# Optimization experiments

Hardware: AMD Instinct MI355X
Metric: run time of the kernel (lower is better)

The kernel has to match this reference:

```python
import jax, jax.numpy as jnp
import numpy as np
import math

D_MODEL = 1024
N_HEADS = 16
FACTOR = 5


def setup_inputs() -> dict:
    key = jax.random.key(0)
    ks = jax.random.split(key, 8)
    B, L, S, d = 8, 4096, 4096, D_MODEL
    sc = 1.0 / math.sqrt(d)
    perm = jnp.asarray(np.random.default_rng(0).permutation(L), jnp.int32)
    return {
        "queries": jax.random.normal(ks[0], (B, L, d), jnp.float32),
        "keys": jax.random.normal(ks[1], (B, S, d), jnp.float32),
        "values": jax.random.normal(ks[2], (B, S, d), jnp.float32),
        "perm": perm,
        "Wq": jax.random.normal(ks[3], (d, d), jnp.float32) * sc,
        "bq": jnp.zeros((d,), jnp.float32),
        "Wk": jax.random.normal(ks[4], (d, d), jnp.float32) * sc,
        "bk": jnp.zeros((d,), jnp.float32),
        "Wv": jax.random.normal(ks[5], (d, d), jnp.float32) * sc,
        "bv": jnp.zeros((d,), jnp.float32),
        "Wo": jax.random.normal(ks[6], (d, d), jnp.float32) * sc,
        "bo": jnp.zeros((d,), jnp.float32),
    }


def reference(queries, keys, values, perm, Wq, bq, Wk, bk, Wv, bv, Wo, bo):
    B, L, d = queries.shape
    S = keys.shape[1]
    H = N_HEADS
    dk = d // H

    q = (queries @ Wq + bq).reshape(B, L, H, dk)
    k = (keys @ Wk + bk).reshape(B, S, H, dk)
    v = (values @ Wv + bv).reshape(B, S, H, dk)

    # ProbSparse: u = min(factor * ceil(log(S)), L)  (static, shape-derived)
    u_part = FACTOR * int(math.ceil(math.log(S)))
    u = min(u_part, L)

    # sample u queries (perm replaces torch.randperm for determinism)
    q_sample = q[:, perm[:u]]                                   # [B,u,H,dk]
    scores_sample = jnp.einsum('buhd,bshd->bhus', q_sample, k)  # [B,H,u,S]

    # sparsity measurement M = max_s - mean_s
    M = scores_sample.max(-1) - scores_sample.sum(-1) / S       # [B,H,u]
    _, M_top = jax.lax.top_k(M, u)                              # [B,H,u] indices in [0,u)

    # gather top-u queries per (batch, head) along the L axis
    qT = q.transpose(0, 2, 1, 3)                                # [B,H,L,dk]
    q_red = jnp.take_along_axis(qT, M_top[..., None], axis=2)   # [B,H,u,dk]

    scores = jnp.einsum('bhud,bshd->bhus', q_red, k)            # [B,H,u,S]
    attn = jax.nn.softmax(scores, axis=-1)
    context = jnp.einsum('bhus,bshd->buhd', attn, v).reshape(B, u, d)
    output = context @ Wo + bo                                  # [B,u,d]
    return output, attn
```

## Files before the change

kernel.cpp:

```cpp
#include <hip/hip_runtime.h>
#include <stdint.h>
#include <stddef.h>

#define DEV static __device__ __forceinline__

typedef short short8 __attribute__((ext_vector_type(8)));
typedef short short4v __attribute__((ext_vector_type(4)));
typedef float f32x4 __attribute__((ext_vector_type(4)));
typedef _Float16 half8 __attribute__((ext_vector_type(8)));

DEV uint16_t f2h(float x){
  union { _Float16 h; uint16_t u; } c; c.h = (_Float16)x; return c.u;
}

DEV f32x4 mfma16h(short8 a, short8 b, f32x4 c){
  union { short8 s; half8 h; } ua, ub; ua.s = a; ub.s = b;
  return __builtin_amdgcn_mfma_f32_16x16x32_f16(ua.h, ub.h, c, 0, 0, 0);
}

typedef const __attribute__((address_space(1))) void* gas1;
typedef __attribute__((address_space(3))) void* las3;
DEV void async16(const void* g, void* l){
  __builtin_amdgcn_global_load_lds((gas1)g, (las3)l, 16, 0, 0);
}

DEV int swzoct(int row, int oct){ return (oct & ~7) | ((oct ^ row) & 7); }
DEV short8 lds_frag(const short* base, int row, int rowOcts, int oct){
  int o = swzoct(row, oct);
  return *(const short8*)(base + row * rowOcts * 8 + o * 8);
}
DEV void lds_store8(short* base, int row, int rowOcts, int oct, short8 v){
  int o = swzoct(row, oct);
  *(short8*)(base + row * rowOcts * 8 + o * 8) = v;
}

__global__ __launch_bounds__(256) void pa_prep_weights(
    const float* __restrict__ Wk, const float* __restrict__ Wv,
    uint16_t* WkT, uint16_t* WvT){
  int which = blockIdx.y;
  const float* W = which ? Wv : Wk;
  uint16_t* O = which ? WvT : WkT;
  int e0 = (blockIdx.x * 256 + threadIdx.x) * 4;
  #pragma unroll
  for(int c=0;c<4;c++){
    int e = e0 + c; int n = e >> 10, k = e & 1023;
    O[e] = f2h(W[(size_t)k*1024 + n]);
  }
}

__global__ __launch_bounds__(256) void pa_prep_inputs(
    const float* __restrict__ keys, const float* __restrict__ values,
    uint16_t* __restrict__ kf, uint16_t* __restrict__ vf){
  size_t e = ((size_t)blockIdx.x * 256 + threadIdx.x) * 8;
  const float* src = blockIdx.y ? values : keys;
  uint16_t* dst = blockIdx.y ? vf : kf;
  float4 u0 = *(const float4*)(src + e);
  float4 u1 = *(const float4*)(src + e + 4);
  float xs[8] = {u0.x,u0.y,u0.z,u0.w,u1.x,u1.y,u1.z,u1.w};
  short8 hv;
  #pragma unroll
  for(int c=0;c<8;c++) hv[c] = (short)f2h(xs[c]);
  *(short8*)(dst + e) = hv;
}

__global__ __launch_bounds__(256) void pa_q_stage1(
    const float* __restrict__ queries, const int* __restrict__ perm,
    const float* __restrict__ Wq, double* __restrict__ qpart){
  __shared__ alignas(16) float Alds[96*32];
  __shared__ alignas(16) float Blds[32*128];
  int ct = blockIdx.x, kc = blockIdx.y, b = blockIdx.z;
  int t = threadIdx.x;
  int tr = t >> 4, tc = t & 15;
  const float* qb = queries + (size_t)b*4096*1024;
  const float* srcA[3];
  #pragma unroll
  for(int rr=0; rr<3; rr++){
    int chunk = rr*256 + t;
    int row = chunk >> 3, c8 = chunk & 7;
    int rid = (row < 45) ? perm[row] : (row < 90 ? row - 45 : 0);
    srcA[rr] = qb + (size_t)rid*1024 + c8*4;
  }
  const float* srcB[4];
  #pragma unroll
  for(int rr=0; rr<4; rr++){
    int chunk = rr*256 + t;
    int kk = chunk >> 5, c = chunk & 31;
    srcB[rr] = Wq + (size_t)kk*1024 + ct*128 + c*4;
  }
  double acc[6][8];
  #pragma unroll
  for(int i=0;i<6;i++)
    #pragma unroll
    for(int jj=0;jj<8;jj++) acc[i][jj] = 0.0;
  int k0 = kc*128;
  for(int ks=0; ks<4; ks++){
    int kk0 = k0 + ks*32;
    #pragma unroll
    for(int rr=0; rr<3; rr++)
      async16(srcA[rr] + kk0, (char*)Alds + (rr*256 + t)*16);
    #pragma unroll
    for(int rr=0; rr<4; rr++)
      async16(srcB[rr] + (size_t)kk0*1024, (char*)Blds + (rr*256 + t)*16);
    __syncthreads();
    #pragma unroll
    for(int kk=0; kk<32; kk++){
      double av[6];
      #pragma unroll
      for(int i=0;i<6;i++) av[i] = (double)Alds[(tr*6+i)*32 + kk];
      float4 b0 = *(const float4*)(Blds + kk*128 + tc*8);
      float4 b1 = *(const float4*)(Blds + kk*128 + tc*8 + 4);
      double bv[8] = {(double)b0.x,(double)b0.y,(double)b0.z,(double)b0.w,
                      (double)b1.x,(double)b1.y,(double)b1.z,(double)b1.w};
      #pragma unroll
      for(int i=0;i<6;i++)
        #pragma unroll
        for(int jj=0;jj<8;jj++)
          acc[i][jj] += av[i]*bv[jj];
    }
    __syncthreads();
  }
  #pragma unroll
  for(int i=0;i<6;i++){
    int r = tr*6 + i;
    double* dst = qpart + (((size_t)b*96 + r)*8 + kc)*1024 + ct*128 + tc*8;
    #pragma unroll
    for(int jj=0;jj<8;jj++) dst[jj] = acc[i][jj];
  }
}

__global__ __launch_bounds__(256) void pa_q_finalize(
    const double* __restrict__ qpart, const float* __restrict__ bq,
    float* q_f32, uint16_t* q_f16){
  int slot = blockIdx.x, b = blockIdx.y;
  int j = (slot < 45) ? slot : ((slot >= 48 && slot < 93) ? (45 + slot - 48) : -1);
  #pragma unroll
  for(int c=0;c<4;c++){
    int n = threadIdx.x * 4 + c;
    float v = 0.f;
    if(j >= 0){
      const double* p = qpart + (((size_t)b*96 + j)*8)*1024 + n;
      double s = 0.0;
      #pragma unroll
      for(int kc=0;kc<8;kc++) s += p[(size_t)kc*1024];
      v = (float)(s + (double)bq[n]);
    }
    int h = n >> 6, d = n & 63;
    size_t idx = (((size_t)(b*16 + h))*96 + slot)*64 + d;
    q_f32[idx] = v;
    q_f16[idx] = f2h(v);
  }
}

template<bool TR>
__global__ __launch_bounds__(256) void pa_kv_gemm(
    const uint16_t* __restrict__ Ag, const uint16_t* __restrict__ Bg,
    const float* __restrict__ bias, uint16_t* __restrict__ out){
  __shared__ alignas(16) short Ah[128*64], Bh[128*64];
  int tid = threadIdx.x, wid = tid >> 6, lane = tid & 63;
  int bid = blockIdx.x;
  int xcd = bid & 7, slot = bid >> 3;
  int mt = xcd*32 + (slot >> 3), nt = slot & 7;
  int m0 = mt*128, n0 = nt*128;
  int rsub = lane >> 3;
  int soct = (lane & 7) ^ rsub;
  const uint16_t* a0 = Ag + (size_t)(m0 + wid*32 + rsub)*1024 + soct*8;
  const uint16_t* b0 = Bg + (size_t)(n0 + wid*32 + rsub)*1024 + soct*8;
  short* lA = Ah + wid*32*64;
  short* lB = Bh + wid*32*64;
  f32x4 acc[4][4];
  #pragma unroll
  for(int i=0;i<4;i++)
    #pragma unroll
    for(int jj=0;jj<4;jj++) acc[i][jj] = (f32x4){0.f,0.f,0.f,0.f};
  int wr = wid >> 1, wc = wid & 1;
  for(int kb=0; kb<16; kb++){
    int ko = kb*64;
    #pragma unroll
    for(int q=0;q<4;q++){
      async16(a0 + ko + q*8*1024, lA + q*512);
      async16(b0 + ko + q*8*1024, lB + q*512);
    }
    __syncthreads();
    short8 Af[4][2];
    #pragma unroll
    for(int mf=0;mf<4;mf++)
      #pragma unroll
      for(int k2=0;k2<2;k2++){
        int row = wr*64 + mf*16 + (lane & 15);
        int oct = k2*4 + (lane >> 4);
        Af[mf][k2] = lds_frag(Ah, row, 8, oct);
      }
    #pragma unroll
    for(int nf=0;nf<4;nf++){
      short8 Bf[2];
      #pragma unroll
      for(int k2=0;k2<2;k2++){
        int row = wc*64 + nf*16 + (lane & 15);
        int oct = k2*4 + (lane >> 4);
        Bf[k2] = lds_frag(Bh, row, 8, oct);
      }
      #pragma unroll
      for(int mf=0;mf<4;mf++)
        #pragma unroll
        for(int k2=0;k2<2;k2++)
          acc[mf][nf] = mfma16h(Af[mf][k2], Bf[k2], acc[mf][nf]);
    }
    __syncthreads();
  }
  int b = m0 >> 12, s_base = m0 & 4095;
  #pragma unroll
  for(int mf=0;mf<4;mf++)
    #pragma unroll
    for(int nf=0;nf<4;nf++){
      int srow = s_base + wr*64 + mf*16 + ((lane >> 4) << 2);
      int ncol = n0 + wc*64 + nf*16 + (lane & 15);
      float bia = bias[ncol];
      int h = ncol >> 6, d = ncol & 63;
      if constexpr(!TR){
        size_t base = ((((size_t)(b*16 + h))*4096 + srow)*64 + d);
        #pragma unroll
        for(int i=0;i<4;i++)
          out[base + (size_t)i*64] = f2h(acc[mf][nf][i] + bia);
      } else {
        short4v pk;
        #pragma unroll
        for(int i=0;i<4;i++) pk[i] = (short)f2h(acc[mf][nf][i] + bia);
        *(short4v*)(out + ((((size_t)(b*16 + h))*64 + d)*4096 + srow)) = pk;
      }
    }
}

__global__ __launch_bounds__(256) void pa_p1_stats(
    const uint16_t* __restrict__ q_f16, const uint16_t* __restrict__ khg,
    float* __restrict__ stats){
  __shared__ alignas(16) short qf[96*64], kh[128*64];
  int chunk = blockIdx.x, h = blockIdx.y, b = blockIdx.z;
  int tid = threadIdx.x, wid = tid >> 6, lane = tid & 63;
  const uint16_t* qsf = q_f16 + ((size_t)(b*16 + h))*96*64;
  #pragma unroll
  for(int jj=0;jj<3;jj++){
    int oc = tid*3 + jj;
    int sl = oc >> 3, o = oc & 7;
    lds_store8(qf, sl, 8, o, *(const short8*)(qsf + sl*64 + o*8));
  }
  float t1v[3][4], t2v[3][4], t3v[3][4], ssum[3][4], mm[3][4], zz[3][4];
  int t1i[3][4], t2i[3][4], t3i[3][4];
  #pragma unroll
  for(int a=0;a<3;a++)
    #pragma unroll
    for(int i=0;i<4;i++){
      t1v[a][i]=-3e38f; t2v[a][i]=-3e38f; t3v[a][i]=-3e38f; ssum[a][i]=0.f;
      mm[a][i]=-3e38f; zz[a][i]=0.f; t1i[a][i]=0; t2i[a][i]=0; t3i[a][i]=0;
    }
  int rsub = lane >> 3, soct = (lane & 7) ^ rsub;
  const uint16_t* khb = khg + (((size_t)(b*16 + h))*4096)*64;
  __syncthreads();
  for(int st=0; st<4; st++){
    int sg0 = chunk*512 + st*128;
    #pragma unroll
    for(int q=0;q<4;q++){
      int row = wid*32 + q*8;
      async16(khb + (size_t)(sg0 + row + rsub)*64 + soct*8, kh + row*64);
    }
    __syncthreads();
    short8 Bf[2][2];
    #pragma unroll
    for(int nf=0;nf<2;nf++)
      #pragma unroll
      for(int k2=0;k2<2;k2++){
        int scol = wid*32 + nf*16 + (lane & 15);
        int oct = k2*4 + (lane >> 4);
        Bf[nf][k2] = lds_frag(kh, scol, 8, oct);
      }
    #pragma unroll
    for(int mf=0;mf<6;mf++){
      short8 af[2];
      #pragma unroll
      for(int k2=0;k2<2;k2++){
        int row = mf*16 + (lane & 15);
        int oct = k2*4 + (lane >> 4);
        af[k2] = lds_frag(qf, row, 8, oct);
      }
      f32x4 a0 = (f32x4){0.f,0.f,0.f,0.f}, a1 = a0;
      #pragma unroll
      for(int k2=0;k2<2;k2++){
        a0 = mfma16h(af[k2], Bf[0][k2], a0);
        a1 = mfma16h(af[k2], Bf[1][k2], a1);
      }
      #pragma unroll
      for(int nf=0;nf<2;nf++){
        int sgl = sg0 + wid*32 + nf*16 + (lane & 15);
        #pragma unroll
        for(int i=0;i<4;i++){
          float v = nf ? a1[i] : a0[i];
          if(mf < 3){
            ssum[mf][i] += v;
            if(v > t1v[mf][i]){
              t3v[mf][i]=t2v[mf][i]; t3i[mf][i]=t2i[mf][i];
              t2v[mf][i]=t1v[mf][i]; t2i[mf][i]=t1i[mf][i];
              t1v[mf][i]=v; t1i[mf][i]=sgl;
            } else if(v > t2v[mf][i]){
              t3v[mf][i]=t2v[mf][i]; t3i[mf][i]=t2i[mf][i];
              t2v[mf][i]=v; t2i[mf][i]=sgl;
            } else if(v > t3v[mf][i]){
              t3v[mf][i]=v; t3i[mf][i]=sgl;
            }
          } else {
            int q = mf - 3;
            float mn = fmaxf(mm[q][i], v);
            zz[q][i] = zz[q][i]*__expf(mm[q][i]-mn) + __expf(v-mn);
            mm[q][i] = mn;
          }
        }
      }
    }
    __syncthreads();
  }
  size_t sbase = (((((size_t)b*16 + h)*8 + chunk)*4 + wid)*96)*8;
  #pragma unroll
  for(int mf=0;mf<3;mf++)
    #pragma unroll
    for(int i=0;i<4;i++){
      float v1=t1v[mf][i], v2=t2v[mf][i], v3=t3v[mf][i], sm=ssum[mf][i];
      int i1=t1i[mf][i], i2=t2i[mf][i], i3=t3i[mf][i];
      #pragma unroll
      for(int msk=1; msk<16; msk<<=1){
        float w1=__shfl_xor(v1,msk,64), w2=__shfl_xor(v2,msk,64), w3=__shfl_xor(v3,msk,64);
        int j1=__shfl_xor(i1,msk,64), j2=__shfl_xor(i2,msk,64), j3=__shfl_xor(i3,msk,64);
        sm += __shfl_xor(sm,msk,64);
        if(w1 > v1){
          float tv; int ti;
          tv=v1; v1=w1; w1=tv; ti=i1; i1=j1; j1=ti;
          tv=v2; v2=w2; w2=tv; ti=i2; i2=j2; j2=ti;
          tv=v3; v3=w3; w3=tv; ti=i3; i3=j3; j3=ti;
        }
        if(w1 > v2){
          v3=v2; i3=i2; v2=w1; i2=j1;
          if(w2 > v3){ v3=w2; i3=j2; }
        } else if(w1 > v3){ v3=w1; i3=j1; }
      }
      if((lane & 15) == 0){
        int sl = mf*16 + ((lane >> 4) << 2) + i;
        float* dst = stats + sbase + (size_t)sl*8;
        dst[0]=v1; dst[1]=__int_as_float(i1); dst[2]=v2; dst[3]=__int_as_float(i2);
        dst[4]=v3; dst[5]=__int_as_float(i3); dst[6]=sm;
      }
    }
  #pragma unroll
  for(int q=0;q<3;q++)
    #pragma unroll
    for(int i=0;i<4;i++){
      float m1=mm[q][i], z1=zz[q][i];
      #pragma unroll
      for(int msk=1; msk<16; msk<<=1){
        float m2=__shfl_xor(m1,msk,64), z2=__shfl_xor(z1,msk,64);
        float mn = fmaxf(m1,m2);
        z1 = z1*__expf(m1-mn) + z2*__expf(m2-mn);
        m1 = mn;
      }
      if((lane & 15) == 0){
        int sl = 48 + q*16 + ((lane >> 4) << 2) + i;
        float* dst = stats + sbase + (size_t)sl*8;
        dst[0]=m1; dst[1]=z1;
      }
    }
}

__global__ __launch_bounds__(256) void pa_sort_mark(
    const float* __restrict__ stats,
    float* __restrict__ mzfin,
    float* __restrict__ Mv_g, float* __restrict__ Ssum_g,
    int* __restrict__ mlist_g, int* __restrict__ clist_g,
    int* __restrict__ nmark_g){
  int h = blockIdx.x, b = blockIdx.y;
  int bh = b*16 + h;
  __shared__ float Mv[48], Ssum[48];
  __shared__ int I1[48], I2[48], I3[48];
  __shared__ int order[48], mlist[48], flags[48];
  __shared__ int clist[144];
  __shared__ int nmark;
  int t = threadIdx.x;
  const float* sb = stats + (((size_t)bh)*8*4*96)*8;
  if(t < 48) flags[t] = 0;
  if(t < 48){
    float v1=-3e38f, v2=-3e38f, v3=-3e38f, sm=0.f; int i1=0, i2=0, i3=0;
    for(int c=0;c<8;c++)
      for(int w=0;w<4;w++){
        const float* p = sb + (((size_t)c*4 + w)*96 + t)*8;
        float w1=p[0], w2=p[2], w3=p[4];
        int j1=__float_as_int(p[1]), j2=__float_as_int(p[3]), j3=__float_as_int(p[5]);
        sm += p[6];
        if(w1 > v1){
          float tv; int ti;
          tv=v1; v1=w1; w1=tv; ti=i1; i1=j1; j1=ti;
          tv=v2; v2=w2; w2=tv; ti=i2; i2=j2; j2=ti;
          tv=v3; v3=w3; w3=tv; ti=i3; i3=j3; j3=ti;
        }
        if(w1 > v2){
          v3=v2; i3=i2; v2=w1; i2=j1;
          if(w2 > v3){ v3=w2; i3=j2; }
        } else if(w1 > v3){ v3=w1; i3=j1; }
      }
    Mv[t] = v1 - sm*(1.0f/4096.0f);
    I1[t]=i1; I2[t]=i2; I3[t]=i3; Ssum[t]=sm;
  }
  if(t >= 64 && t < 112){
    int i = t - 64;
    float m1=-3e38f, z1=0.f;
    for(int c=0;c<8;c++)
      for(int w=0;w<4;w++){
        const float* p = sb + (((size_t)c*4 + w)*96 + 48 + i)*8;
        float m2=p[0], z2=p[1];
        float mn = fmaxf(m1,m2);
        z1 = z1*__expf(m1-mn) + z2*__expf(m2-mn);
        m1 = mn;
      }
    mzfin[((size_t)bh*48 + i)*2 + 0] = m1;
    mzfin[((size_t)bh*48 + i)*2 + 1] = z1;
  }
  __syncthreads();
  if(t < 64){
    float v = (t < 45) ? Mv[t] : -3e38f;
    int rank = 0;
    #pragma unroll
    for(int j=0;j<45;j++){
      float vj = __shfl(v, j, 64);
      rank += (vj > v) || (vj == v && j < (int)t);
    }
    if(t < 45) order[rank] = t;
  }
  __syncthreads();
  if(t < 44){
    if(Mv[order[t]] - Mv[order[t+1]] < 0.025f){
      flags[order[t]] = 1; flags[order[t+1]] = 1;
    }
  }
  __syncthreads();
  if(t == 0){
    int cnt=0;
    for(int i=0;i<45;i++) if(flags[i]){
      clist[3*cnt]   = I1[i];
      clist[3*cnt+1] = I2[i];
      clist[3*cnt+2] = I3[i];
      mlist[cnt++]=i;
    }
    nmark = cnt;
  }
  __syncthreads();
  int nm = nmark;
  if(t < 48){
    Mv_g[(size_t)bh*48 + t] = Mv[t];
    Ssum_g[(size_t)bh*48 + t] = Ssum[t];
  }
  if(t < nm) mlist_g[(size_t)bh*48 + t] = mlist[t];
  if(t < 3*nm) clist_g[(size_t)bh*144 + t] = clist[t];
  if(t == 0) nmark_g[bh] = nm;
}

__global__ __launch_bounds__(256) void pa_refine(
    const float* __restrict__ keys, const float* __restrict__ Wk,
    const float* __restrict__ q_f32,
    const int* __restrict__ mlist_g, const int* __restrict__ clist_g,
    const int* __restrict__ nmark_g, double* __restrict__ scx_g){
  int cid = blockIdx.x, h = blockIdx.y, b = blockIdx.z;
  int bh = b*16 + h;
  int nc = nmark_g[bh]*3;
  if(cid >= nc) return;
  __shared__ double red[256];
  int t = threadIdx.x;
  int kq = t >> 6, d = t & 63;
  int sidx = clist_g[(size_t)bh*144 + cid];
  int u = mlist_g[(size_t)bh*48 + cid/3];
  const float* krow = keys + ((size_t)b*4096 + sidx)*1024;
  double acc = 0.0;
  int col = h*64 + d;
  #pragma unroll 8
  for(int k=kq*256; k<kq*256+256; k++)
    acc += (double)krow[k] * (double)Wk[(size_t)k*1024 + col];
  red[t] = acc;
  __syncthreads();
  if(t < 64){
    double kd = red[t] + red[64+t] + red[128+t] + red[192+t];
    double sp = kd * (double)q_f32[((size_t)bh*96 + u)*64 + t];
    #pragma unroll
    for(int m=1; m<64; m<<=1) sp += __shfl_xor(sp, m, 64);
    if(t == 0) scx_g[(size_t)bh*144 + cid] = sp;
  }
}

__global__ __launch_bounds__(64) void pa_final_rank(
    const float* __restrict__ Mv_g, const float* __restrict__ Ssum_g,
    const int* __restrict__ mlist_g, const int* __restrict__ nmark_g,
    const double* __restrict__ scx_g, int* __restrict__ invrk){
  int h = blockIdx.x, b = blockIdx.y;
  int bh = b*16 + h;
  __shared__ float Mv[48];
  int t = threadIdx.x;
  if(t < 48) Mv[t] = Mv_g[(size_t)bh*48 + t];
  int nm = nmark_g[bh];
  __syncthreads();
  if(t < nm){
    int u = mlist_g[(size_t)bh*48 + t];
    const double* s3 = scx_g + (size_t)bh*144 + 3*t;
    double mx = s3[0];
    if(s3[1] > mx) mx = s3[1];
    if(s3[2] > mx) mx = s3[2];
    Mv[u] = (float)mx - Ssum_g[(size_t)bh*48 + u]*(1.0f/4096.0f);
  }
  __syncthreads();
  float v = (t < 45) ? Mv[t] : -3e38f;
  int rank = 0;
  #pragma unroll
  for(int j=0;j<45;j++){
    float vj = __shfl(v, j, 64);
    rank += (vj > v) || (vj == v && j < (int)t);
  }
  if(t < 45) invrk[(size_t)bh*48 + t] = rank;
}

__global__ __launch_bounds__(256) void pa_p2_attn(
    const uint16_t* __restrict__ q_f16, const uint16_t* __restrict__ khg,
    const uint16_t* __restrict__ v_t,
    const float* __restrict__ mzfin, const int* __restrict__ invrk,
    float* __restrict__ attn_out, float* __restrict__ ctx2){
  __shared__ alignas(16) short qf[48*64];
  __shared__ alignas(16) short kh[64*64];
  __shared__ alignas(16) short vT[64*64];
  __shared__ alignas(16) short Pl[48*64];
  int chunk = blockIdx.x, h = blockIdx.y, b = blockIdx.z;
  int tid = threadIdx.x, wid = tid >> 6, lane = tid & 63;
  const uint16_t* qsf = q_f16 + (((size_t)(b*16 + h))*96 + 48)*64;
  for(int oc=tid; oc<384; oc+=256){
    int sl = oc >> 3, o = oc & 7;
    lds_store8(qf, sl, 8, o, *(const short8*)(qsf + sl*64 + o*8));
  }
  float mreg[3][4], invz[3][4];
  int rrk[3][4];
  #pragma unroll
  for(int mf=0;mf<3;mf++)
    #pragma unroll
    for(int i=0;i<4;i++){
      int u = mf*16 + ((lane >> 4) << 2) + i;
      mreg[mf][i] = mzfin[(((size_t)(b*16 + h))*48 + u)*2 + 0];
      invz[mf][i] = 1.f / mzfin[(((size_t)(b*16 + h))*48 + u)*2 + 1];
      rrk[mf][i] = invrk[((size_t)(b*16 + h))*48 + u];
    }
  f32x4 ctx[3];
  #pragma unroll
  for(int mf=0;mf<3;mf++) ctx[mf] = (f32x4){0.f,0.f,0.f,0.f};
  int rsub = lane >> 3, soct = (lane & 7) ^ rsub;
  const uint16_t* khb = khg + (((size_t)(b*16 + h))*4096)*64;
  const uint16_t* vtb = v_t + (((size_t)(b*16 + h))*64)*4096;
  __syncthreads();
  for(int st=0; st<8; st++){
    int sg0 = chunk*512 + st*64;
    #pragma unroll
    for(int q=0;q<2;q++){
      int row = wid*16 + q*8;
      async16(khb + (size_t)(sg0 + row + rsub)*64 + soct*8, kh + row*64);
      async16(vtb + (size_t)(row + rsub)*4096 + sg0 + soct*8, vT + row*64);
    }
    __syncthreads();
    short8 Bf[2];
    #pragma unroll
    for(int k2=0;k2<2;k2++){
      int scol = wid*16 + (lane & 15);
      int oct = k2*4 + (lane >> 4);
      Bf[k2] = lds_frag(kh, scol, 8, oct);
    }
    #pragma unroll
    for(int mf=0;mf<3;mf++){
      short8 af[2];
      #pragma unroll
      for(int k2=0;k2<2;k2++){
        int row = mf*16 + (lane & 15);
        int oct = k2*4 + (lane >> 4);
        af[k2] = lds_frag(qf, row, 8, oct);
      }
      f32x4 a0 = (f32x4){0.f,0.f,0.f,0.f};
      #pragma unroll
      for(int k2=0;k2<2;k2++)
        a0 = mfma16h(af[k2], Bf[k2], a0);
      int scl = wid*16 + (lane & 15);
      #pragma unroll
      for(int i=0;i<4;i++){
        int u = mf*16 + ((lane >> 4) << 2) + i;
        float p = __expf(a0[i] - mreg[mf][i]) * invz[mf][i];
        if(u < 45){
          attn_out[(((size_t)(b*16 + h))*45 + rrk[mf][i])*4096 + sg0 + scl] = p;
        }
        int oct = scl >> 3;
        int o = (oct ^ (u & 7)) & 7;
        Pl[u*64 + o*8 + (scl & 7)] = (short)f2h(p);
      }
    }
    __syncthreads();
    #pragma unroll
    for(int k2=0;k2<2;k2++){
      int oct = k2*4 + (lane >> 4);
      int drow = wid*16 + (lane & 15);
      short8 bv = lds_frag(vT, drow, 8, oct);
      #pragma unroll
      for(int mf=0;mf<3;mf++){
        int row = mf*16 + (lane & 15);
        short8 ap = lds_frag(Pl, row, 8, oct);
        ctx[mf] = mfma16h(ap, bv, ctx[mf]);
      }
    }
    __syncthreads();
  }
  #pragma unroll
  for(int mf=0;mf<3;mf++)
    #pragma unroll
    for(int i=0;i<4;i++){
      int u = mf*16 + ((lane >> 4) << 2) + i;
      if(u < 45){
        int d = wid*16 + (lane & 15);
        ctx2[(((size_t)chunk*8 + b)*45 + rrk[mf][i])*1024 + h*64 + d] = ctx[mf][i];
      }
    }
}

__global__ __launch_bounds__(256) void pa_out_gemm(
    const float* __restrict__ ctx2, const float* __restrict__ Wo,
    const float* __restrict__ bo, float* __restrict__ out){
  __shared__ float cl[8][1024];
  int bx = blockIdx.x, by = blockIdx.y;
  int t = threadIdx.x;
  for(int e=t; e<8*1024; e+=256){
    int rr = e >> 10, k = e & 1023;
    size_t grow = (size_t)by*8 + rr;
    float s = 0.f;
    #pragma unroll
    for(int c=0;c<8;c++) s += ctx2[((size_t)c*360 + grow)*1024 + k];
    cl[rr][k] = s;
  }
  __syncthreads();
  int quad = t & 63, rg = t >> 6;
  int n = bx*256 + quad*4;
  float acc[2][4];
  #pragma unroll
  for(int rr=0;rr<2;rr++)
    #pragma unroll
    for(int c=0;c<4;c++) acc[rr][c]=0.f;
  for(int k=0;k<1024;k++){
    float4 w = *(const float4*)(Wo + (size_t)k*1024 + n);
    float c0 = cl[rg*2][k], c1 = cl[rg*2+1][k];
    acc[0][0] += c0*w.x; acc[0][1] += c0*w.y; acc[0][2] += c0*w.z; acc[0][3] += c0*w.w;
    acc[1][0] += c1*w.x; acc[1][1] += c1*w.y; acc[1][2] += c1*w.z; acc[1][3] += c1*w.w;
  }
  #pragma unroll
  for(int rr=0;rr<2;rr++){
    size_t grow = (size_t)by*8 + rg*2 + rr;
    #pragma unroll
    for(int c=0;c<4;c++) out[grow*1024 + n + c] = acc[rr][c] + bo[n + c];
  }
}

extern "C" void kernel_launch(void* const* d_in, const int* in_sizes, int n_in,
                              void* d_out, int out_size, void* d_ws, size_t ws_size,
                              hipStream_t stream){
  const float* queries = (const float*)d_in[0];
  const float* keys    = (const float*)d_in[1];
  const float* values  = (const float*)d_in[2];
  const int*   perm    = (const int*)d_in[3];
  const float* Wq = (const float*)d_in[4]; const float* bq = (const float*)d_in[5];
  const float* Wk = (const float*)d_in[6]; const float* bk = (const float*)d_in[7];
  const float* Wv = (const float*)d_in[8]; const float* bv = (const float*)d_in[9];
  const float* Wo = (const float*)d_in[10]; const float* bo = (const float*)d_in[11];

  char* ws = (char*)d_ws;
  const size_t SZ = (size_t)33554432;
  uint16_t* kf_in = (uint16_t*)(ws);
  uint16_t* vf_in = (uint16_t*)(ws + SZ*2);
  uint16_t* k_o   = (uint16_t*)(ws + SZ*4);
  uint16_t* v_t   = (uint16_t*)(ws + SZ*6);
  uint16_t* WkT   = (uint16_t*)(ws + SZ*8);
  uint16_t* WvT   = (uint16_t*)(ws + SZ*8 + 2097152);
  float*    q_f32 = (float*)   (ws + SZ*8 + 4194304);
  uint16_t* q_f16 = (uint16_t*)(ws + SZ*8 + 7340032);

  char* rg = ws + SZ*2;
  double* qpart   = (double*)rg;
  float*  stats   = (float*)rg;
  float*  mzfin   = (float*)(rg + 12582912);
  int*    invrk   = (int*)  (rg + 12632064);
  float*  ctx2    = (float*)(rg + 12656640);
  float*  Mv_g    = (float*)(rg + 24453120);
  float*  Ssum_g  = (float*)(rg + 24477696);
  int*    mlist_g = (int*)  (rg + 24502272);
  int*    clist_g = (int*)  (rg + 24526848);
  int*    nmark_g = (int*)  (rg + 24600576);
  double* scx_g   = (double*)(rg + 24601088);

  float* out  = (float*)d_out;
  float* attn = out + (size_t)360*1024;

  pa_prep_weights<<<dim3(1024,2), 256, 0, stream>>>(Wk, Wv, WkT, WvT);
  pa_q_stage1<<<dim3(8,8,8), 256, 0, stream>>>(queries, perm, Wq, qpart);
  pa_q_finalize<<<dim3(96,8), 256, 0, stream>>>(qpart, bq, q_f32, q_f16);
  pa_prep_inputs<<<dim3(16384,2), 256, 0, stream>>>(keys, values, kf_in, vf_in);
  pa_kv_gemm<false><<<2048, 256, 0, stream>>>(kf_in, WkT, bk, k_o);
  pa_kv_gemm<true><<<2048, 256, 0, stream>>>(vf_in, WvT, bv, v_t);
  pa_p1_stats<<<dim3(8,16,8), 256, 0, stream>>>(q_f16, k_o, stats);
  pa_sort_mark<<<dim3(16,8), 256, 0, stream>>>(stats, mzfin, Mv_g, Ssum_g, mlist_g, clist_g, nmark_g);
  pa_refine<<<dim3(135,16,8), 256, 0, stream>>>(keys, Wk, q_f32, mlist_g, clist_g, nmark_g, scx_g);
  pa_final_rank<<<dim3(16,8), 64, 0, stream>>>(Mv_g, Ssum_g, mlist_g, nmark_g, scx_g, invrk);
  pa_p2_attn<<<dim3(8,16,8), 256, 0, stream>>>(q_f16, k_o, v_t, mzfin, invrk, attn, ctx2);
  pa_out_gemm<<<dim3(4,45), 256, 0, stream>>>(ctx2, Wo, bo, out);
}
```

Baseline: 637.3 us.

## Fuse fp32-to-fp16 K/V conversion into GEMM, merge K/V launches, split-K output GEMM

Removes the separate pass that converts keys and values to fp16. The K/V projection GEMM now reads fp32 inputs directly and converts them while staging into LDS, which avoids writing and re-reading 128MB of fp16 intermediates. The K and V GEMMs run in one launch selected by blockIdx.y. The output projection is split four ways over K into a partial kernel plus a reduce kernel, to raise parallelism above 180 blocks. The A operand is now loaded synchronously instead of with async LDS loads, so load/compute overlap may drop and register pressure may rise.

```diff
diff --git a/kernel.cpp b/kernel.cpp
--- a/kernel.cpp
+++ b/kernel.cpp
@@ -46,21 +46,6 @@
     int e = e0 + c; int n = e >> 10, k = e & 1023;
     O[e] = f2h(W[(size_t)k*1024 + n]);
   }
-}
-
-__global__ __launch_bounds__(256) void pa_prep_inputs(
-    const float* __restrict__ keys, const float* __restrict__ values,
-    uint16_t* __restrict__ kf, uint16_t* __restrict__ vf){
-  size_t e = ((size_t)blockIdx.x * 256 + threadIdx.x) * 8;
-  const float* src = blockIdx.y ? values : keys;
-  uint16_t* dst = blockIdx.y ? vf : kf;
-  float4 u0 = *(const float4*)(src + e);
-  float4 u1 = *(const float4*)(src + e + 4);
-  float xs[8] = {u0.x,u0.y,u0.z,u0.w,u1.x,u1.y,u1.z,u1.w};
-  short8 hv;
-  #pragma unroll
-  for(int c=0;c<8;c++) hv[c] = (short)f2h(xs[c]);
-  *(short8*)(dst + e) = hv;
 }
 
 __global__ __launch_bounds__(256) void pa_q_stage1(
@@ -151,11 +136,16 @@
   }
 }
 
-template<bool TR>
 __global__ __launch_bounds__(256) void pa_kv_gemm(
-    const uint16_t* __restrict__ Ag, const uint16_t* __restrict__ Bg,
-    const float* __restrict__ bias, uint16_t* __restrict__ out){
+    const float* __restrict__ keys, const float* __restrict__ values,
+    const uint16_t* __restrict__ WkT, const uint16_t* __restrict__ WvT,
+    const float* __restrict__ bk, const float* __restrict__ bv,
+    uint16_t* __restrict__ k_o, uint16_t* __restrict__ v_t){
   __shared__ alignas(16) short Ah[128*64], Bh[128*64];
+  const bool TR = (blockIdx.y == 1);
+  const float* Ag = TR ? values : keys;
+  const uint16_t* Bg = TR ? WvT : WkT;
+  const float* bias = TR ? bv : bk;
   int tid = threadIdx.x, wid = tid >> 6, lane = tid & 63;
   int bid = blockIdx.x;
   int xcd = bid & 7, slot = bid >> 3;
@@ -163,7 +153,7 @@
   int m0 = mt*128, n0 = nt*128;
   int rsub = lane >> 3;
   int soct = (lane & 7) ^ rsub;
-  const uint16_t* a0 = Ag + (size_t)(m0 + wid*32 + rsub)*1024 + soct*8;
+  const float*    aF = Ag + (size_t)(m0 + wid*32 + rsub)*1024 + soct*8;
   const uint16_t* b0 = Bg + (size_t)(n0 + wid*32 + rsub)*1024 + soct*8;
   short* lA = Ah + wid*32*64;
   short* lB = Bh + wid*32*64;
@@ -176,9 +166,19 @@
   for(int kb=0; kb<16; kb++){
     int ko = kb*64;
     #pragma unroll
+    for(int q=0;q<4;q++)
+      async16(b0 + ko + q*8*1024, lB + q*512);
+    #pragma unroll
     for(int q=0;q<4;q++){
-      async16(a0 + ko + q*8*1024, lA + q*512);
-      async16(b0 + ko + q*8*1024, lB + q*512);
+      const float* src = aF + ko + (size_t)q*8*1024;
+      float4 u0 = *(const float4*)(src);
+      float4 u1 = *(const float4*)(src + 4);
+      short8 hv;
+      hv[0]=(short)f2h(u0.x); hv[1]=(short)f2h(u0.y);
+      hv[2]=(short)f2h(u0.z); hv[3]=(short)f2h(u0.w);
+      hv[4]=(short)f2h(u1.x); hv[5]=(short)f2h(u1.y);
+      hv[6]=(short)f2h(u1.z); hv[7]=(short)f2h(u1.w);
+      *(short8*)(lA + q*512 + lane*8) = hv;
     }
     __syncthreads();
     short8 Af[4][2];
@@ -216,16 +216,16 @@
       int ncol = n0 + wc*64 + nf*16 + (lane & 15);
       float bia = bias[ncol];
       int h = ncol >> 6, d = ncol & 63;
-      if constexpr(!TR){
+      if(!TR){
         size_t base = ((((size_t)(b*16 + h))*4096 + srow)*64 + d);
         #pragma unroll
         for(int i=0;i<4;i++)
-          out[base + (size_t)i*64] = f2h(acc[mf][nf][i] + bia);
+          k_o[base + (size_t)i*64] = f2h(acc[mf][nf][i] + bia);
       } else {
         short4v pk;
         #pragma unroll
         for(int i=0;i<4;i++) pk[i] = (short)f2h(acc[mf][nf][i] + bia);
-        *(short4v*)(out + ((((size_t)(b*16 + h))*64 + d)*4096 + srow)) = pk;
+        *(short4v*)(v_t + ((((size_t)(b*16 + h))*64 + d)*4096 + srow)) = pk;
       }
     }
 }
@@ -621,19 +621,19 @@
     }
 }
 
-__global__ __launch_bounds__(256) void pa_out_gemm(
+__global__ __launch_bounds__(256) void pa_out_part(
     const float* __restrict__ ctx2, const float* __restrict__ Wo,
-    const float* __restrict__ bo, float* __restrict__ out){
-  __shared__ float cl[8][1024];
-  int bx = blockIdx.x, by = blockIdx.y;
+    float* __restrict__ opart){
+  __shared__ float cl[8][256];
+  int bx = blockIdx.x, by = blockIdx.y, kc = blockIdx.z;
   int t = threadIdx.x;
-  for(int e=t; e<8*1024; e+=256){
-    int rr = e >> 10, k = e & 1023;
+  for(int e=t; e<8*256; e+=256){
+    int rr = e >> 8, kk = e & 255;
     size_t grow = (size_t)by*8 + rr;
     float s = 0.f;
     #pragma unroll
-    for(int c=0;c<8;c++) s += ctx2[((size_t)c*360 + grow)*1024 + k];
-    cl[rr][k] = s;
+    for(int c=0;c<8;c++) s += ctx2[((size_t)c*360 + grow)*1024 + kc*256 + kk];
+    cl[rr][kk] = s;
   }
   __syncthreads();
   int quad = t & 63, rg = t >> 6;
@@ -643,8 +643,8 @@
   for(int rr=0;rr<2;rr++)
     #pragma unroll
     for(int c=0;c<4;c++) acc[rr][c]=0.f;
-  for(int k=0;k<1024;k++){
-    float4 w = *(const float4*)(Wo + (size_t)k*1024 + n);
+  for(int k=0;k<256;k++){
+    float4 w = *(const float4*)(Wo + (size_t)(kc*256 + k)*1024 + n);
     float c0 = cl[rg*2][k], c1 = cl[rg*2+1][k];
     acc[0][0] += c0*w.x; acc[0][1] += c0*w.y; acc[0][2] += c0*w.z; acc[0][3] += c0*w.w;
     acc[1][0] += c1*w.x; acc[1][1] += c1*w.y; acc[1][2] += c1*w.z; acc[1][3] += c1*w.w;
@@ -653,8 +653,19 @@
   for(int rr=0;rr<2;rr++){
     size_t grow = (size_t)by*8 + rg*2 + rr;
     #pragma unroll
-    for(int c=0;c<4;c++) out[grow*1024 + n + c] = acc[rr][c] + bo[n + c];
-  }
+    for(int c=0;c<4;c++)
+      opart[((size_t)kc*360 + grow)*1024 + n + c] = acc[rr][c];
+  }
+}
+
+__global__ __launch_bounds__(256) void pa_out_reduce(
+    const float* __restrict__ opart, const float* __restrict__ bo,
+    float* __restrict__ out){
+  size_t e = (size_t)blockIdx.x*256 + threadIdx.x;
+  const size_t N = (size_t)360*1024;
+  if(e >= N) return;
+  float s = ((opart[e] + opart[e + N]) + opart[e + 2*N]) + opart[e + 3*N];
+  out[e] = s + bo[e & 1023];
 }
 
 extern "C" void kernel_launch(void* const* d_in, const int* in_sizes, int n_in,
@@ -671,8 +682,6 @@
 
   char* ws = (char*)d_ws;
   const size_t SZ = (size_t)33554432;
-  uint16_t* kf_in = (uint16_t*)(ws);
-  uint16_t* vf_in = (uint16_t*)(ws + SZ*2);
   uint16_t* k_o   = (uint16_t*)(ws + SZ*4);
   uint16_t* v_t   = (uint16_t*)(ws + SZ*6);
   uint16_t* WkT   = (uint16_t*)(ws + SZ*8);
@@ -692,6 +701,7 @@
   int*    clist_g = (int*)  (rg + 24526848);
   int*    nmark_g = (int*)  (rg + 24600576);
   double* scx_g   = (double*)(rg + 24601088);
+  float*  opart   = (float*)(rg + 24748544);
 
   float* out  = (float*)d_out;
   float* attn = out + (size_t)360*1024;
@@ -699,13 +709,12 @@
   pa_prep_weights<<<dim3(1024,2), 256, 0, stream>>>(Wk, Wv, WkT, WvT);
   pa_q_stage1<<<dim3(8,8,8), 256, 0, stream>>>(queries, perm, Wq, qpart);
   pa_q_finalize<<<dim3(96,8), 256, 0, stream>>>(qpart, bq, q_f32, q_f16);
-  pa_prep_inputs<<<dim3(16384,2), 256, 0, stream>>>(keys, values, kf_in, vf_in);
-  pa_kv_gemm<false><<<2048, 256, 0, stream>>>(kf_in, WkT, bk, k_o);
-  pa_kv_gemm<true><<<2048, 256, 0, stream>>>(vf_in, WvT, bv, v_t);
+  pa_kv_gemm<<<dim3(2048,2), 256, 0, stream>>>(keys, values, WkT, WvT, bk, bv, k_o, v_t);
   pa_p1_stats<<<dim3(8,16,8), 256, 0, stream>>>(q_f16, k_o, stats);
   pa_sort_mark<<<dim3(16,8), 256, 0, stream>>>(stats, mzfin, Mv_g, Ssum_g, mlist_g, clist_g, nmark_g);
   pa_refine<<<dim3(135,16,8), 256, 0, stream>>>(keys, Wk, q_f32, mlist_g, clist_g, nmark_g, scx_g);
   pa_final_rank<<<dim3(16,8), 64, 0, stream>>>(Mv_g, Ssum_g, mlist_g, nmark_g, scx_g, invrk);
   pa_p2_attn<<<dim3(8,16,8), 256, 0, stream>>>(q_f16, k_o, v_t, mzfin, invrk, attn, ctx2);
-  pa_out_gemm<<<dim3(4,45), 256, 0, stream>>>(ctx2, Wo, bo, out);
-}
+  pa_out_part<<<dim3(4,45,4), 256, 0, stream>>>(ctx2, Wo, opart);
+  pa_out_reduce<<<1440, 256, 0, stream>>>(opart, bo, out);
+}
```

After: 563.5 us (median of 3 runs). -11.6%, faster.
